# Optimization experiments

Hardware: AMD Instinct MI355X
Metric: run time of the kernel (lower is better)

## Reference

```python
import jax, jax.numpy as jnp
import numpy as np

PAD = 2  # kernel_height // 2 for kernel_height=5


def earth_pad2d(x, ph, pw):
    # circular pad in longitude (last dim), zero pad in latitude (dim 2)
    if pw > 0:
        x = jnp.concatenate([x[..., -pw:], x, x[..., :pw]], axis=-1)
    if ph > 0:
        x = jnp.pad(x, ((0, 0), (0, 0), (ph, ph), (0, 0)))
    return x


def earth_wrap2d(x, w, pad):
    # fold circular overhang of a transposed-conv output back onto width w
    core = x[..., pad:pad + w]
    rw = x.shape[-1] - pad - w  # right overhang (stride-1... here 1)
    core = core.at[..., :rw].add(x[..., pad + w:])
    core = core.at[..., w - pad:].add(x[..., :pad])
    return core


def _conv(x, w, b, stride):
    # torch Conv2d, weight [Cout, Cin, 1, k], VALID padding, stride (1, stride)
    y = jax.lax.conv_general_dilated(x, w, (1, stride), 'VALID',
                                     dimension_numbers=('NCHW', 'OIHW', 'NCHW'))
    return y + b[None, :, None, None]


def _convT(x, w, stride):
    # torch ConvTranspose2d (no bias), weight [Cin, Cout, 1, k], padding 0
    k = w.shape[-1]
    wr = jnp.transpose(jnp.flip(w, axis=(2, 3)), (1, 0, 2, 3))  # -> [Cout, Cin, 1, k]
    return jax.lax.conv_general_dilated(x, wr, (1, 1),
                                        [(0, 0), (k - 1, k - 1)],
                                        lhs_dilation=(1, stride),
                                        dimension_numbers=('NCHW', 'OIHW', 'NCHW'))


def _edge(x, d, p):
    return x[:, :, -p:, :] if d == 1 else x[:, :, :p, :]


def _set_edge(x, d, p, v):
    return x.at[:, :, -p:, :].set(v) if d == 1 else x.at[:, :, :p, :].set(v)


def _forward(strips, wi, wo):
    strips_pad = [earth_pad2d(s, PAD, PAD) for s in strips]
    # center strip inner edges from the adjacent coarser strips (to_inners[0])
    for d in (-1, 1):
        a = _edge(strips[2 + d], -d, PAD)
        a = _convT(a, wi[0], 2)
        a = earth_wrap2d(a, strips[2].shape[3], 2)
        a = earth_pad2d(a, 0, PAD)
        strips_pad[2] = _set_edge(strips_pad[2], d, PAD, a)
    # outer strips: far edge from next coarser (to_inners), near edge from finer (to_outers)
    for mi in (1, 2):
        for d in (-1, 1):
            idx = 2 + d * mi
            sp = strips_pad[idx]
            if mi + 1 <= 2:
                o = _edge(strips[2 + d * (mi + 1)], -d, PAD)
                o = _convT(o, wi[mi], 2)
                o = earth_wrap2d(o, strips[idx].shape[3], 2)
                o = earth_pad2d(o, 0, PAD)
                sp = _set_edge(sp, d, PAD, o)
            en = _edge(strips[2 + d * (mi - 1)], d, PAD)
            en = earth_pad2d(en, 0, 2)
            en = _conv(en, wo[mi - 1][0], wo[mi - 1][1], 2)
            en = earth_pad2d(en, 0, PAD)
            sp = _set_edge(sp, -d, PAD, en)
            strips_pad[idx] = sp
    return tuple(strips_pad)


def setup_inputs():
    key = jax.random.key(0)
    ks = jax.random.split(key, 11)
    B, C, W = 1, 256, 1440
    shapes = [(B, C, 30, W // 4), (B, C, 60, W // 2), (B, C, 180, W),
              (B, C, 60, W // 2), (B, C, 30, W // 4)]
    d = {}
    for i, sh in enumerate(shapes):
        d['s%d' % i] = jax.random.normal(ks[i], sh, dtype=jnp.float32)
    scale = 0.03
    d['wi0'] = jax.random.normal(ks[5], (C, C, 1, 5), dtype=jnp.float32) * scale
    d['wi1'] = jax.random.normal(ks[6], (C, C, 1, 5), dtype=jnp.float32) * scale
    d['wo0'] = jax.random.normal(ks[7], (C, C, 1, 5), dtype=jnp.float32) * scale
    d['bo0'] = jax.random.normal(ks[8], (C,), dtype=jnp.float32) * 0.01
    d['wo1'] = jax.random.normal(ks[9], (C, C, 1, 5), dtype=jnp.float32) * scale
    d['bo1'] = jax.random.normal(ks[10], (C,), dtype=jnp.float32) * 0.01
    return d


def reference(s0, s1, s2, s3, s4, wi0, wi1, wo0, bo0, wo1, bo1):
    return _forward([s0, s1, s2, s3, s4], [wi0, wi1], [(wo0, bo0), (wo1, bo1)])
```

## Files before the change

### kernel.cpp

```cpp
#include <hip/hip_runtime.h>


struct ConvJob {
  const float* x; const float* wt; const float* bias; float* out;
  int Hin, Win, r0, Hout, Wcore, h0, blk_start;
};
struct ConvParams { ConvJob j[8]; };

struct CopyParams {
  const float* in0; const float* in1; const float* in2; const float* in3; const float* in4;
  float* o0; float* o1; float* o2; float* o3; float* o4;
};

struct WTParams { const float* src[4]; float* dst[4]; };

__global__ __launch_bounds__(256) void transpose_all_kernel(WTParams p) {
  int b = blockIdx.x;
  int which = b / 1280;
  int idx = (b - which * 1280) * 256 + threadIdx.x;
  int oc = idx & 255;
  int q = idx >> 8;
  int k = q % 5;
  int ic = q / 5;
  const float* s = p.src[which];
  float v = (which < 2) ? s[(ic * 256 + oc) * 5 + k] : s[(oc * 256 + ic) * 5 + k];
  p.dst[which][idx] = v;
}


template <int NOUT, int NCC>
__device__ __forceinline__ void fma_cols(float* acc, const float* w, const float* xsrow,
                                         int ic0) {
#pragma unroll
  for (int cc = 0; cc < NCC; ++cc) {
    float4 xq = *(const float4*)&xsrow[cc * 256 + ic0];
#pragma unroll
    for (int i = 0; i < NOUT; ++i) {
      int k = (NOUT == 8) ? (cc - 2 * i) : (i + 4 - 2 * cc);
      if (k >= 0 && k < 5)
        acc[i] += w[k] * xq.x + w[5 + k] * xq.y + w[10 + k] * xq.z + w[15 + k] * xq.w;
    }
  }
}

template <int NOUT, int NCC>
__device__ __forceinline__ void conv_unit(const ConvJob jb, int local, int t, float* xs,
                                          float bv) {
  int tile = local >> 1;
  int r = local & 1;
  const int Win = jb.Win;
  const float* xrow = jb.x + ((size_t)(t * jb.Hin + jb.r0 + r)) * Win;
  const float* wt = jb.wt + t;
  const int Wop = jb.Wcore + 4;
  float* orow = jb.out + ((size_t)(t * jb.Hout + jb.h0 + r)) * Wop;

  int base0;
  if (NOUT == 8) base0 = 2 * (tile * 8) - 2;
  else           base0 = (tile * 16 >> 1) - 1;
#pragma unroll
  for (int cc = 0; cc < NCC; ++cc) {
    int col = base0 + cc;
    col += (col < 0) ? Win : 0;
    col -= (col >= Win) ? Win : 0;
    xs[cc * 256 + t] = xrow[col];
  }
  __syncthreads();

  float acc[NOUT];
#pragma unroll
  for (int i = 0; i < NOUT; ++i) acc[i] = bv;

#pragma unroll 1
  for (int ic0 = 0; ic0 < 256; ic0 += 4) {
    float w[20];
#pragma unroll
    for (int e = 0; e < 20; ++e) w[e] = wt[(size_t)(ic0 * 5 + e) * 256];
    fma_cols<NOUT, NCC>(acc, w, xs, ic0);
  }

  int g0 = (NOUT == 8) ? tile * 8 : tile * 16;
#pragma unroll
  for (int i = 0; i < NOUT; ++i) {
    int g = g0 + i;
    float vv = acc[i];
    orow[2 + g] = vv;
    if (g < 2) orow[jb.Wcore + 2 + g] = vv;
    if (g >= jb.Wcore - 2) orow[g - (jb.Wcore - 2)] = vv;
  }
}

__global__ __launch_bounds__(256, 4) void conv_kernel(ConvParams p) {
  __shared__ float xs[19 * 256];
  int bx = blockIdx.x;
  int t = threadIdx.x;
  if (bx < 540) {
    int ji = (bx >= 450) ? 3 : (bx >= 360) ? 2 : (bx >= 180) ? 1 : 0;
    conv_unit<16, 10>(p.j[ji], bx - p.j[ji].blk_start, t, xs, 0.f);
  } else {
    int j2 = (bx >= 990) ? 7 : (bx >= 900) ? 6 : (bx >= 720) ? 5 : 4;
    conv_unit<8, 19>(p.j[j2], bx - p.j[j2].blk_start, t, xs, p.j[j2].bias[t]);
  }
}


__device__ __forceinline__ float4 pack4(float2 a, float2 b) {
  return make_float4(a.x, a.y, b.x, b.y);
}

template <int H, int W>
__device__ __forceinline__ void copy_row(const float* __restrict__ in,
                                         float* __restrict__ out, int rl, int lane) {
  constexpr int CORE = W / 4;
  int c = rl / H;
  const float* src = in + (size_t)rl * W;
  float* dst = out + (size_t)(rl + c * 4 + 2) * (W + 4);
  int w4 = 1 + lane;
  while (w4 < CORE) {
    int w4b = w4 + 64;
    float2 a0 = *(const float2*)(src + w4 * 4 - 2);
    float2 b0 = *(const float2*)(src + w4 * 4);
    if (w4b < CORE) {
      float2 a1 = *(const float2*)(src + w4b * 4 - 2);
      float2 b1 = *(const float2*)(src + w4b * 4);
      *(float4*)(dst + w4 * 4) = pack4(a0, b0);
      *(float4*)(dst + w4b * 4) = pack4(a1, b1);
    } else {
      *(float4*)(dst + w4 * 4) = pack4(a0, b0);
    }
    w4 += 128;
  }
  if (lane == 0) {
    float2 E = *(const float2*)(src + W - 2);
    float2 F = *(const float2*)(src);
    float4 v = pack4(E, F);
    *(float4*)(dst) = v;
    *(float4*)(dst + W) = v;
  }
}

__device__ __forceinline__ void zero_row(const CopyParams& p, int z, int lane) {
  int strip = z >> 9, cr = z & 511, c = cr >> 1, r = cr & 1;
  float* dst = strip ? p.o4 + (size_t)(c * 34 + 32 + r) * 364
                     : p.o0 + (size_t)(c * 34 + r) * 364;
  for (int w4 = lane; w4 < 91; w4 += 64)
    *(float4*)(dst + w4 * 4) = make_float4(0.f, 0.f, 0.f, 0.f);
}

__device__ __forceinline__ void do_row(const CopyParams& p, int gid, int lane) {
  if (gid < 46080)      copy_row<180, 1440>(p.in2, p.o2, gid, lane);
  else if (gid < 61440) copy_row<60, 720>(p.in1, p.o1, gid - 46080, lane);
  else if (gid < 76800) copy_row<60, 720>(p.in3, p.o3, gid - 61440, lane);
  else if (gid < 84480) copy_row<30, 360>(p.in0, p.o0, gid - 76800, lane);
  else if (gid < 92160) copy_row<30, 360>(p.in4, p.o4, gid - 84480, lane);
  else                  zero_row(p, gid - 92160, lane);
}

__global__ __launch_bounds__(256, 8) void copy_kernel(CopyParams p) {
  int wid = blockIdx.x * 4 + (threadIdx.x >> 6);
  int lane = threadIdx.x & 63;
  for (int gid = wid; gid < 93184; gid += 8192) do_row(p, gid, lane);
}

extern "C" void kernel_launch(void* const* d_in, const int* in_sizes, int n_in,
                              void* d_out, int out_size, void* d_ws, size_t ws_size,
                              hipStream_t stream) {
  const float* s0 = (const float*)d_in[0];
  const float* s1 = (const float*)d_in[1];
  const float* s2 = (const float*)d_in[2];
  const float* s3 = (const float*)d_in[3];
  const float* s4 = (const float*)d_in[4];
  const float* wi0 = (const float*)d_in[5];
  const float* wi1 = (const float*)d_in[6];
  const float* wo0 = (const float*)d_in[7];
  const float* bo0 = (const float*)d_in[8];
  const float* wo1 = (const float*)d_in[9];
  const float* bo1 = (const float*)d_in[10];

  float* out = (float*)d_out;
  float* out0 = out;
  float* out1 = out + 3168256;
  float* out2 = out + 15030272;
  float* out3 = out + 83048448;
  float* out4 = out + 94910464;

  float* wt0 = (float*)d_ws;
  float* wt1 = wt0 + 327680;
  float* wt2 = wt1 + 327680;
  float* wt3 = wt2 + 327680;

  WTParams wp;
  wp.src[0] = wi0; wp.src[1] = wi1; wp.src[2] = wo0; wp.src[3] = wo1;
  wp.dst[0] = wt0; wp.dst[1] = wt1; wp.dst[2] = wt2; wp.dst[3] = wt3;
  transpose_all_kernel<<<5120, 256, 0, stream>>>(wp);

  ConvParams cp;
  cp.j[0] = {s1, wt0, nullptr, out2,  60,  720,  58, 184, 1440,   0,   0};
  cp.j[1] = {s3, wt0, nullptr, out2,  60,  720,   0, 184, 1440, 182, 180};
  cp.j[2] = {s0, wt1, nullptr, out1,  30,  360,  28,  64,  720,   0, 360};
  cp.j[3] = {s4, wt1, nullptr, out3,  30,  360,   0,  64,  720,  62, 450};
  cp.j[4] = {s2, wt2, bo0,     out1, 180, 1440,   0,  64,  720,  62, 540};
  cp.j[5] = {s2, wt2, bo0,     out3, 180, 1440, 178,  64,  720,   0, 720};
  cp.j[6] = {s1, wt3, bo1,     out0,  60,  720,   0,  34,  360,  32, 900};
  cp.j[7] = {s3, wt3, bo1,     out4,  60,  720,  58,  34,  360,   0, 990};
  conv_kernel<<<1080, 256, 0, stream>>>(cp);

  CopyParams kp;
  kp.in0 = s0; kp.in1 = s1; kp.in2 = s2; kp.in3 = s3; kp.in4 = s4;
  kp.o0 = out0; kp.o1 = out1; kp.o2 = out2; kp.o3 = out3; kp.o4 = out4;
  copy_kernel<<<2048, 256, 0, stream>>>(kp);
}
```

Before: 335.4 us.

## Vectorize weight loads via interleaved layout and coalesce output stores through LDS

Reorders the transposed weight buffer so each output channel holds 4 consecutive input channels per tap. Each thread can then fetch weights with five float4 loads per group instead of twenty scalar strided loads. The output is staged in shared memory and written as coalesced float2 stores along the width dimension, replacing per-thread scattered writes to separate rows. This adds two barriers and extra LDS traffic, and the halo wrap writes are handled separately.

```diff
diff --git a/kernel.cpp b/kernel.cpp
--- a/kernel.cpp
+++ b/kernel.cpp
@@ -18,30 +18,18 @@
   int b = blockIdx.x;
   int which = b / 1280;
   int idx = (b - which * 1280) * 256 + threadIdx.x;
-  int oc = idx & 255;
-  int q = idx >> 8;
-  int k = q % 5;
-  int ic = q / 5;
+  int hi = idx >> 10;
+  int icq = hi / 5;
+  int k = hi - icq * 5;
+  int lo = idx & 1023;
+  int oc = lo >> 2;
+  int icr = lo & 3;
+  int ic = icq * 4 + icr;
   const float* s = p.src[which];
   float v = (which < 2) ? s[(ic * 256 + oc) * 5 + k] : s[(oc * 256 + ic) * 5 + k];
   p.dst[which][idx] = v;
 }
 
-
-template <int NOUT, int NCC>
-__device__ __forceinline__ void fma_cols(float* acc, const float* w, const float* xsrow,
-                                         int ic0) {
-#pragma unroll
-  for (int cc = 0; cc < NCC; ++cc) {
-    float4 xq = *(const float4*)&xsrow[cc * 256 + ic0];
-#pragma unroll
-    for (int i = 0; i < NOUT; ++i) {
-      int k = (NOUT == 8) ? (cc - 2 * i) : (i + 4 - 2 * cc);
-      if (k >= 0 && k < 5)
-        acc[i] += w[k] * xq.x + w[5 + k] * xq.y + w[10 + k] * xq.z + w[15 + k] * xq.w;
-    }
-  }
-}
 
 template <int NOUT, int NCC>
 __device__ __forceinline__ void conv_unit(const ConvJob jb, int local, int t, float* xs,
@@ -49,14 +37,15 @@
   int tile = local >> 1;
   int r = local & 1;
   const int Win = jb.Win;
+  const int Hout = jb.Hout;
   const float* xrow = jb.x + ((size_t)(t * jb.Hin + jb.r0 + r)) * Win;
-  const float* wt = jb.wt + t;
+  const float* wq = jb.wt + t * 4;
   const int Wop = jb.Wcore + 4;
-  float* orow = jb.out + ((size_t)(t * jb.Hout + jb.h0 + r)) * Wop;
+  float* orow = jb.out + ((size_t)(t * Hout + jb.h0 + r)) * Wop;
 
   int base0;
   if (NOUT == 8) base0 = 2 * (tile * 8) - 2;
-  else           base0 = (tile * 16 >> 1) - 1;
+  else           base0 = tile * 8 - 1;
 #pragma unroll
   for (int cc = 0; cc < NCC; ++cc) {
     int col = base0 + cc;
@@ -71,21 +60,48 @@
   for (int i = 0; i < NOUT; ++i) acc[i] = bv;
 
 #pragma unroll 1
-  for (int ic0 = 0; ic0 < 256; ic0 += 4) {
-    float w[20];
-#pragma unroll
-    for (int e = 0; e < 20; ++e) w[e] = wt[(size_t)(ic0 * 5 + e) * 256];
-    fma_cols<NOUT, NCC>(acc, w, xs, ic0);
-  }
-
+  for (int icq = 0; icq < 64; ++icq) {
+    float4 wv[5];
+#pragma unroll
+    for (int k = 0; k < 5; ++k)
+      wv[k] = *(const float4*)(wq + (size_t)(icq * 5 + k) * 1024);
+    int ic0 = icq * 4;
+#pragma unroll
+    for (int cc = 0; cc < NCC; ++cc) {
+      float4 xq = *(const float4*)&xs[cc * 256 + ic0];
+#pragma unroll
+      for (int i = 0; i < NOUT; ++i) {
+        int k = (NOUT == 8) ? (cc - 2 * i) : (i + 4 - 2 * cc);
+        if (k >= 0 && k < 5) {
+          float4 w = wv[k];
+          acc[i] += w.x * xq.x + w.y * xq.y + w.z * xq.z + w.w * xq.w;
+        }
+      }
+    }
+  }
+
+  __syncthreads();
+#pragma unroll
+  for (int i = 0; i < NOUT; ++i) xs[i * 257 + t] = acc[i];
+  __syncthreads();
+  constexpr int SL = NOUT / 2;
+  constexpr int OCR = 256 / SL;
+  constexpr int RND = 256 / OCR;
   int g0 = (NOUT == 8) ? tile * 8 : tile * 16;
 #pragma unroll
-  for (int i = 0; i < NOUT; ++i) {
-    int g = g0 + i;
-    float vv = acc[i];
-    orow[2 + g] = vv;
-    if (g < 2) orow[jb.Wcore + 2 + g] = vv;
-    if (g >= jb.Wcore - 2) orow[g - (jb.Wcore - 2)] = vv;
+  for (int q = 0; q < RND; ++q) {
+    int oc = (t / SL) + q * OCR;
+    int s = t & (SL - 1);
+    float2 v = make_float2(xs[(2 * s) * 257 + oc], xs[(2 * s + 1) * 257 + oc]);
+    *(float2*)(jb.out + ((size_t)(oc * Hout + jb.h0 + r)) * Wop + 2 + g0 + 2 * s) = v;
+  }
+  if (tile == 0) {
+    orow[jb.Wcore + 2] = xs[0 * 257 + t];
+    orow[jb.Wcore + 3] = xs[1 * 257 + t];
+  }
+  if (g0 + NOUT == jb.Wcore) {
+    orow[0] = xs[(NOUT - 2) * 257 + t];
+    orow[1] = xs[(NOUT - 1) * 257 + t];
   }
 }
 
```

New measurement: 322.6 us. 3.8% less time.
